# Kernel tuning notes

Hardware: AMD Instinct MI355X
Metric: run time of the kernel (lower is better)

Reference implementation:

```python
import jax, jax.numpy as jnp
import numpy as np

BN_EPS = 1e-5


def feature_gather(fmap, xy):
    """Bilinear grid_sample (align_corners=False, zero padding).
    fmap: (B, C, H, W), xy: (B, N, 2) in [-1, 1]. Returns (B, C, N)."""
    B, C, H, W = fmap.shape
    ix = ((xy[..., 0] + 1.0) * W - 1.0) * 0.5  # (B, N)
    iy = ((xy[..., 1] + 1.0) * H - 1.0) * 0.5
    ix0 = jnp.floor(ix); iy0 = jnp.floor(iy)
    ix1 = ix0 + 1.0;     iy1 = iy0 + 1.0
    wx1 = ix - ix0; wx0 = 1.0 - wx1
    wy1 = iy - iy0; wy0 = 1.0 - wy1

    def corner(fx, fy, w):
        valid = (fx >= 0) & (fx < W) & (fy >= 0) & (fy < H)
        xi = jnp.clip(fx, 0, W - 1).astype(jnp.int32)
        yi = jnp.clip(fy, 0, H - 1).astype(jnp.int32)
        # per-batch fancy gather: (C, H, W)[:, yi, xi] -> (C, N)
        vals = jax.vmap(lambda f, y, x: f[:, y, x])(fmap, yi, xi)  # (B, C, N)
        return vals * (w * valid.astype(fmap.dtype))[:, None, :]

    return (corner(ix0, iy0, wx0 * wy0) + corner(ix1, iy0, wx1 * wy0)
            + corner(ix0, iy1, wx0 * wy1) + corner(ix1, iy1, wx1 * wy1))


def bn1d(x, g, b, m, v):
    # x: (B, C, N); eval-mode batchnorm with running stats
    inv = jax.lax.rsqrt(v + BN_EPS)
    return (x - m[None, :, None]) * (g * inv)[None, :, None] + b[None, :, None]


def setup_inputs() -> dict:
    key = jax.random.key(0)
    ks = jax.random.split(key, 24)
    B, IC, PC, RC, OUT, H, W, N = 64, 32, 128, 32, 128, 96, 320, 2048
    s = 0.1
    return {
        "img_map": jax.random.normal(ks[0], (B, IC, H, W), jnp.float32),
        "xy": jax.random.uniform(ks[1], (B, N, 2), jnp.float32, -1.0, 1.0),
        "point_feas": jax.random.normal(ks[2], (B, PC, N), jnp.float32),
        "W_ia_conv": jax.random.normal(ks[3], (PC, IC), jnp.float32) * s,
        "b_ia_conv": jnp.zeros((PC,), jnp.float32),
        "g1": jnp.ones((PC,), jnp.float32),
        "bt1": jnp.zeros((PC,), jnp.float32),
        "m1": jax.random.normal(ks[4], (PC,), jnp.float32) * s,
        "v1": jax.random.uniform(ks[5], (PC,), jnp.float32, 0.5, 1.5),
        "Wf1": jax.random.normal(ks[6], (RC, IC), jnp.float32) * s,
        "bf1": jnp.zeros((RC,), jnp.float32),
        "Wf2": jax.random.normal(ks[7], (RC, PC), jnp.float32) * s,
        "bf2": jnp.zeros((RC,), jnp.float32),
        "Wf3": jax.random.normal(ks[8], (1, RC), jnp.float32) * s,
        "bf3": jnp.zeros((1,), jnp.float32),
        "W_fuse": jax.random.normal(ks[9], (OUT, 2 * PC), jnp.float32) * s,
        "b_fuse": jnp.zeros((OUT,), jnp.float32),
        "g2": jnp.ones((OUT,), jnp.float32),
        "bt2": jnp.zeros((OUT,), jnp.float32),
        "m2": jax.random.normal(ks[10], (OUT,), jnp.float32) * s,
        "v2": jax.random.uniform(ks[11], (OUT,), jnp.float32, 0.5, 1.5),
    }


def reference(img_map, xy, point_feas, W_ia_conv, b_ia_conv, g1, bt1, m1, v1,
              Wf1, bf1, Wf2, bf2, Wf3, bf3, W_fuse, b_fuse, g2, bt2, m2, v2):
    # Feature_Gather: sample image features at projected point locations
    img_feas = feature_gather(img_map, xy)  # (B, IC, N)

    # IA_Layer attention gate
    ri = jnp.einsum('bin,ri->brn', img_feas, Wf1) + bf1[None, :, None]
    rp = jnp.einsum('bpn,rp->brn', point_feas, Wf2) + bf2[None, :, None]
    att = jax.nn.sigmoid(jnp.einsum('brn,or->bon', jnp.tanh(ri + rp), Wf3)
                         + bf3[None, :, None])  # (B, 1, N)

    # IA_Layer conv1: 1x1 conv IC->PC + BN + ReLU, gated by attention
    img_new = jnp.einsum('bin,pi->bpn', img_feas, W_ia_conv) + b_ia_conv[None, :, None]
    img_new = jax.nn.relu(bn1d(img_new, g1, bt1, m1, v1)) * att  # (B, PC, N)

    # Atten_Fusion_Conv: concat + 1x1 conv + BN + ReLU
    fus = jnp.concatenate([point_feas, img_new], axis=1)  # (B, 2*PC, N)
    fus = jnp.einsum('bcn,oc->bon', fus, W_fuse) + b_fuse[None, :, None]
    return jax.nn.relu(bn1d(fus, g2, bt2, m2, v2))  # (B, OUT, N)
```

## Files before the change

### kernel.cpp

```cpp
#include <hip/hip_runtime.h>
#include <math.h>

constexpr int B    = 64;
constexpr int IC   = 32;
constexpr int PC   = 128;
constexpr int RC   = 32;
constexpr int OUTC = 128;
constexpr int H    = 96;
constexpr int IW   = 320;
constexpr int NPT  = 2048;
constexpr float EPS = 1e-5f;

constexpr int BDIM = 256;
constexpr int NT   = 64;

__device__ __forceinline__ float fast_tanh(float v) {
    float e = __expf(2.f * v);
    return 1.f - 2.f / (e + 1.f);
}
__device__ __forceinline__ float fast_sigmoid(float v) {
    return 1.f / (1.f + __expf(-v));
}

__global__ __launch_bounds__(BDIM, 2) void rcnn_fused(
    const float* __restrict__ img_map, const float* __restrict__ xy,
    const float* __restrict__ point_feas,
    const float* __restrict__ Wia, const float* __restrict__ b_ia,
    const float* __restrict__ g1, const float* __restrict__ bt1,
    const float* __restrict__ m1, const float* __restrict__ v1,
    const float* __restrict__ Wf1, const float* __restrict__ bf1,
    const float* __restrict__ Wf2, const float* __restrict__ bf2,
    const float* __restrict__ Wf3, const float* __restrict__ bf3,
    const float* __restrict__ Wfuse, const float* __restrict__ b_fuse,
    const float* __restrict__ g2, const float* __restrict__ bt2,
    const float* __restrict__ m2, const float* __restrict__ v2,
    float* __restrict__ out)
{
    __shared__ float s_if[NT][IC + 1];
    __shared__ float s_Ximg[PC][NT];
    __shared__ float s_Xpf[32][NT];
    __shared__ float s_Wt[32][OUTC + 4];
    __shared__ float s_attp[4][NT];

    const int t  = threadIdx.x;
    const int b  = blockIdx.y;
    const int n0 = blockIdx.x * NT;
    const int p  = t & 63;
    const int q  = t >> 6;
    const int qu = __builtin_amdgcn_readfirstlane(q);
    const int n  = n0 + p;

    {
        float xc = xy[((size_t)b * NPT + n) * 2 + 0];
        float yc = xy[((size_t)b * NPT + n) * 2 + 1];
        float ix = ((xc + 1.f) * (float)IW - 1.f) * 0.5f;
        float iy = ((yc + 1.f) * (float)H  - 1.f) * 0.5f;
        float fx0 = floorf(ix), fy0 = floorf(iy);
        float wx1 = ix - fx0, wx0f = 1.f - wx1;
        float wy1 = iy - fy0, wy0f = 1.f - wy1;
        int x0 = (int)fx0, y0 = (int)fy0;
        int x1 = x0 + 1,  y1 = y0 + 1;
        bool vx0 = (x0 >= 0) && (x0 < IW), vx1 = (x1 >= 0) && (x1 < IW);
        bool vy0 = (y0 >= 0) && (y0 < H),  vy1 = (y1 >= 0) && (y1 < H);
        int cx0 = min(max(x0, 0), IW - 1), cx1 = min(max(x1, 0), IW - 1);
        int cy0 = min(max(y0, 0), H - 1),  cy1 = min(max(y1, 0), H - 1);
        float w00 = wx0f * wy0f * ((vx0 && vy0) ? 1.f : 0.f);
        float w01 = wx1  * wy0f * ((vx1 && vy0) ? 1.f : 0.f);
        float w10 = wx0f * wy1  * ((vx0 && vy1) ? 1.f : 0.f);
        float w11 = wx1  * wy1  * ((vx1 && vy1) ? 1.f : 0.f);
        int o00 = cy0 * IW + cx0, o01 = cy0 * IW + cx1;
        int o10 = cy1 * IW + cx0, o11 = cy1 * IW + cx1;
        const float* fm = img_map + (size_t)b * IC * H * IW + (size_t)(qu * 8) * (H * IW);
        #pragma unroll
        for (int cc = 0; cc < 8; ++cc) {
            const float* f = fm + (size_t)cc * (H * IW);
            s_if[p][qu * 8 + cc] = w00 * f[o00] + w01 * f[o01] + w10 * f[o10] + w11 * f[o11];
        }
    }
    __syncthreads();

    float fre[IC];
    #pragma unroll
    for (int c = 0; c < IC; ++c) fre[c] = s_if[p][c];

    float racc[8];
    #pragma unroll
    for (int i = 0; i < 8; ++i) racc[i] = bf1[qu * 8 + i] + bf2[qu * 8 + i];
    {
        const float* pfb = point_feas + (size_t)b * PC * NPT + n;
        #pragma unroll 4
        for (int c = 0; c < PC; ++c) {
            float pf = pfb[(size_t)c * NPT];
            #pragma unroll
            for (int i = 0; i < 8; ++i)
                racc[i] += Wf2[(qu * 8 + i) * PC + c] * pf;
        }
    }
    #pragma unroll
    for (int c = 0; c < IC; ++c) {
        #pragma unroll
        for (int i = 0; i < 8; ++i)
            racc[i] += Wf1[(qu * 8 + i) * IC + c] * fre[c];
    }
    {
        float apart = 0.f;
        #pragma unroll
        for (int i = 0; i < 8; ++i) apart += Wf3[qu * 8 + i] * fast_tanh(racc[i]);
        s_attp[q][p] = apart;
    }
    __syncthreads();

    {
        float att = fast_sigmoid(s_attp[0][p] + s_attp[1][p] + s_attp[2][p] + s_attp[3][p]
                                 + bf3[0]);
        #pragma unroll
        for (int oo = 0; oo < 32; ++oo) {
            int o = qu * 32 + oo;
            float acc = 0.f;
            #pragma unroll
            for (int c = 0; c < IC; ++c) acc += Wia[o * IC + c] * fre[c];
            float sc  = g1[o] * rsqrtf(v1[o] + EPS);
            float val = (acc + b_ia[o] - m1[o]) * sc + bt1[o];
            s_Ximg[o][p] = fmaxf(val, 0.f) * att;
        }
    }

    const int tn  = t & 15;
    const int to  = t >> 4;
    const int oo0 = to * 8, nn0 = tn * 4;
    float acc[8][4];
    #pragma unroll
    for (int i = 0; i < 8; ++i)
        #pragma unroll
        for (int k = 0; k < 4; ++k) acc[i][k] = 0.f;

    for (int chk = 0; chk < 8; ++chk) {
        const int cb = chk * 32;
        #pragma unroll
        for (int j = 0; j < 16; ++j) {
            int idx = t + j * BDIM;
            int c = idx & 31, o = idx >> 5;
            s_Wt[c][o] = Wfuse[o * 256 + cb + c];
        }
        if (cb < PC) {
            #pragma unroll
            for (int j = 0; j < 8; ++j) {
                int idx = t + j * BDIM;
                int c = idx >> 6, pp = idx & 63;
                s_Xpf[c][pp] = point_feas[((size_t)b * PC + cb + c) * NPT + n0 + pp];
            }
        }
        __syncthreads();

        const float* Xb = (cb < PC) ? &s_Xpf[0][0] : &s_Ximg[cb - PC][0];
        #pragma unroll 4
        for (int c = 0; c < 32; ++c) {
            float4 xv = *(const float4*)(Xb + c * NT + nn0);
            float4 wa = *(const float4*)(&s_Wt[c][oo0]);
            float4 wb = *(const float4*)(&s_Wt[c][oo0 + 4]);
            float wv[8] = {wa.x, wa.y, wa.z, wa.w, wb.x, wb.y, wb.z, wb.w};
            float xr[4] = {xv.x, xv.y, xv.z, xv.w};
            #pragma unroll
            for (int i = 0; i < 8; ++i)
                #pragma unroll
                for (int k = 0; k < 4; ++k)
                    acc[i][k] += wv[i] * xr[k];
        }
        __syncthreads();
    }

    #pragma unroll
    for (int i = 0; i < 8; ++i) {
        int o = oo0 + i;
        float sc = g2[o] * rsqrtf(v2[o] + EPS);
        float bs = (b_fuse[o] - m2[o]) * sc + bt2[o];
        float4 r;
        r.x = fmaxf(acc[i][0] * sc + bs, 0.f);
        r.y = fmaxf(acc[i][1] * sc + bs, 0.f);
        r.z = fmaxf(acc[i][2] * sc + bs, 0.f);
        r.w = fmaxf(acc[i][3] * sc + bs, 0.f);
        *(float4*)(out + ((size_t)b * OUTC + o) * NPT + n0 + nn0) = r;
    }
}

extern "C" void kernel_launch(void* const* d_in, const int* in_sizes, int n_in,
                              void* d_out, int out_size, void* d_ws, size_t ws_size,
                              hipStream_t stream) {
    const float* img_map    = (const float*)d_in[0];
    const float* xy         = (const float*)d_in[1];
    const float* point_feas = (const float*)d_in[2];
    const float* Wia        = (const float*)d_in[3];
    const float* b_ia       = (const float*)d_in[4];
    const float* g1         = (const float*)d_in[5];
    const float* bt1        = (const float*)d_in[6];
    const float* m1         = (const float*)d_in[7];
    const float* v1         = (const float*)d_in[8];
    const float* Wf1        = (const float*)d_in[9];
    const float* bf1        = (const float*)d_in[10];
    const float* Wf2        = (const float*)d_in[11];
    const float* bf2        = (const float*)d_in[12];
    const float* Wf3        = (const float*)d_in[13];
    const float* bf3        = (const float*)d_in[14];
    const float* Wfuse      = (const float*)d_in[15];
    const float* b_fuse     = (const float*)d_in[16];
    const float* g2         = (const float*)d_in[17];
    const float* bt2        = (const float*)d_in[18];
    const float* m2         = (const float*)d_in[19];
    const float* v2         = (const float*)d_in[20];
    float* out = (float*)d_out;

    dim3 grid(NPT / NT, B);
    rcnn_fused<<<grid, BDIM, 0, stream>>>(
        img_map, xy, point_feas, Wia, b_ia, g1, bt1, m1, v1,
        Wf1, bf1, Wf2, bf2, Wf3, bf3, Wfuse, b_fuse, g2, bt2, m2, v2, out);
}
```

Before: 680.8 us.

## Run fusion GEMM on bf16 MFMA with overlapped shared memory and XCD-aware block mapping

Replaces the FP32 scalar-FMA fusion GEMM with bf16 MFMA 16x16x32 instructions. Weights, point features and gated image features are converted to bf16 and stored in shared memory, and several buffers now share one overlay region to cut LDS use. Launch bounds are raised to allow more resident blocks, and the grid is flattened with a mapping that sends each batch to a single XCD for L2 locality. The BN2 scale and bias are precomputed once into shared memory. Rounding GEMM inputs to bf16 reduces precision, and the output stores are now scalar and strided per lane rather than float4.

```diff
diff --git a/kernel.cpp b/kernel.cpp
--- a/kernel.cpp
+++ b/kernel.cpp
@@ -1,10 +1,12 @@
 #include <hip/hip_runtime.h>
 #include <math.h>
+
+typedef __attribute__((ext_vector_type(8))) short short8;
+typedef __attribute__((ext_vector_type(4))) float floatx4;
 
 constexpr int B    = 64;
 constexpr int IC   = 32;
 constexpr int PC   = 128;
-constexpr int RC   = 32;
 constexpr int OUTC = 128;
 constexpr int H    = 96;
 constexpr int IW   = 320;
@@ -14,6 +16,11 @@
 constexpr int BDIM = 256;
 constexpr int NT   = 64;
 
+__device__ __forceinline__ unsigned f2bf(float x) {
+    unsigned u = __builtin_bit_cast(unsigned, x);
+    u += 0x7FFFu + ((u >> 16) & 1u);
+    return u >> 16;
+}
 __device__ __forceinline__ float fast_tanh(float v) {
     float e = __expf(2.f * v);
     return 1.f - 2.f / (e + 1.f);
@@ -22,7 +29,7 @@
     return 1.f / (1.f + __expf(-v));
 }
 
-__global__ __launch_bounds__(BDIM, 2) void rcnn_fused(
+__global__ __launch_bounds__(BDIM, 4) void rcnn_fused(
     const float* __restrict__ img_map, const float* __restrict__ xy,
     const float* __restrict__ point_feas,
     const float* __restrict__ Wia, const float* __restrict__ b_ia,
@@ -36,19 +43,31 @@
     const float* __restrict__ m2, const float* __restrict__ v2,
     float* __restrict__ out)
 {
-    __shared__ float s_if[NT][IC + 1];
-    __shared__ float s_Ximg[PC][NT];
-    __shared__ float s_Xpf[32][NT];
-    __shared__ float s_Wt[32][OUTC + 4];
-    __shared__ float s_attp[4][NT];
-
-    const int t  = threadIdx.x;
-    const int b  = blockIdx.y;
-    const int n0 = blockIdx.x * NT;
-    const int p  = t & 63;
-    const int q  = t >> 6;
-    const int qu = __builtin_amdgcn_readfirstlane(q);
-    const int n  = n0 + p;
+    __shared__ __align__(16) short s_Ximg[NT][136];
+    __shared__ __align__(16) char s_ovl[15360];
+    __shared__ float s_sc[OUTC], s_bs[OUTC];
+
+    short (*s_Wc)[40]  = (short(*)[40])s_ovl;
+    short (*s_Xpf)[40] = (short(*)[40])(s_ovl + 10240);
+    float (*s_if)[33]  = (float(*)[33])s_ovl;
+    float (*s_attp)[NT]= (float(*)[NT])(s_ovl + 8448);
+
+    const int t    = threadIdx.x;
+    const int bid  = blockIdx.x;
+    const int xcd  = bid & 7;
+    const int rr   = bid >> 3;
+    const int b    = (xcd << 3) | (rr >> 5);
+    const int n0   = (rr & 31) * NT;
+    const int lane = t & 63;
+    const int w    = t >> 6;
+    const int wq   = __builtin_amdgcn_readfirstlane(w);
+    const int n    = n0 + lane;
+
+    if (t < OUTC) {
+        float sc = g2[t] * rsqrtf(v2[t] + EPS);
+        s_sc[t] = sc;
+        s_bs[t] = (b_fuse[t] - m2[t]) * sc + bt2[t];
+    }
 
     {
         float xc = xy[((size_t)b * NPT + n) * 2 + 0];
@@ -70,116 +89,125 @@
         float w11 = wx1  * wy1  * ((vx1 && vy1) ? 1.f : 0.f);
         int o00 = cy0 * IW + cx0, o01 = cy0 * IW + cx1;
         int o10 = cy1 * IW + cx0, o11 = cy1 * IW + cx1;
-        const float* fm = img_map + (size_t)b * IC * H * IW + (size_t)(qu * 8) * (H * IW);
+        const float* fm = img_map + (size_t)b * IC * H * IW + (size_t)(wq * 8) * (H * IW);
         #pragma unroll
         for (int cc = 0; cc < 8; ++cc) {
             const float* f = fm + (size_t)cc * (H * IW);
-            s_if[p][qu * 8 + cc] = w00 * f[o00] + w01 * f[o01] + w10 * f[o10] + w11 * f[o11];
+            s_if[lane][wq * 8 + cc] = w00 * f[o00] + w01 * f[o01] + w10 * f[o10] + w11 * f[o11];
         }
     }
     __syncthreads();
 
     float fre[IC];
     #pragma unroll
-    for (int c = 0; c < IC; ++c) fre[c] = s_if[p][c];
-
-    float racc[8];
-    #pragma unroll
-    for (int i = 0; i < 8; ++i) racc[i] = bf1[qu * 8 + i] + bf2[qu * 8 + i];
+    for (int c = 0; c < IC; ++c) fre[c] = s_if[lane][c];
+
     {
+        float racc[8];
+        #pragma unroll
+        for (int i = 0; i < 8; ++i) racc[i] = bf1[wq * 8 + i] + bf2[wq * 8 + i];
         const float* pfb = point_feas + (size_t)b * PC * NPT + n;
         #pragma unroll 4
         for (int c = 0; c < PC; ++c) {
             float pf = pfb[(size_t)c * NPT];
             #pragma unroll
             for (int i = 0; i < 8; ++i)
-                racc[i] += Wf2[(qu * 8 + i) * PC + c] * pf;
-        }
-    }
+                racc[i] += Wf2[(wq * 8 + i) * PC + c] * pf;
+        }
+        #pragma unroll
+        for (int c = 0; c < IC; ++c) {
+            #pragma unroll
+            for (int i = 0; i < 8; ++i)
+                racc[i] += Wf1[(wq * 8 + i) * IC + c] * fre[c];
+        }
+        float apart = 0.f;
+        #pragma unroll
+        for (int i = 0; i < 8; ++i) apart += Wf3[wq * 8 + i] * fast_tanh(racc[i]);
+        s_attp[w][lane] = apart;
+    }
+    __syncthreads();
+
+    {
+        float att = fast_sigmoid(s_attp[0][lane] + s_attp[1][lane] + s_attp[2][lane]
+                                 + s_attp[3][lane] + bf3[0]);
+        #pragma unroll
+        for (int jj = 0; jj < 4; ++jj) {
+            short8 v;
+            #pragma unroll
+            for (int e = 0; e < 8; ++e) {
+                int o = wq * 32 + jj * 8 + e;
+                float acc = 0.f;
+                #pragma unroll
+                for (int c = 0; c < IC; ++c) acc += Wia[o * IC + c] * fre[c];
+                float sc  = g1[o] * rsqrtf(v1[o] + EPS);
+                float val = (acc + b_ia[o] - m1[o]) * sc + bt1[o];
+                val = fmaxf(val, 0.f) * att;
+                v[e] = (short)f2bf(val);
+            }
+            *(short8*)&s_Ximg[lane][wq * 32 + jj * 8] = v;
+        }
+    }
+    __syncthreads();
+
+    const int row16 = lane & 15;
+    const int quad  = lane >> 4;
+    floatx4 acc[2][4];
     #pragma unroll
-    for (int c = 0; c < IC; ++c) {
-        #pragma unroll
-        for (int i = 0; i < 8; ++i)
-            racc[i] += Wf1[(qu * 8 + i) * IC + c] * fre[c];
-    }
-    {
-        float apart = 0.f;
-        #pragma unroll
-        for (int i = 0; i < 8; ++i) apart += Wf3[qu * 8 + i] * fast_tanh(racc[i]);
-        s_attp[q][p] = apart;
-    }
-    __syncthreads();
-
-    {
-        float att = fast_sigmoid(s_attp[0][p] + s_attp[1][p] + s_attp[2][p] + s_attp[3][p]
-                                 + bf3[0]);
-        #pragma unroll
-        for (int oo = 0; oo < 32; ++oo) {
-            int o = qu * 32 + oo;
-            float acc = 0.f;
-            #pragma unroll
-            for (int c = 0; c < IC; ++c) acc += Wia[o * IC + c] * fre[c];
-            float sc  = g1[o] * rsqrtf(v1[o] + EPS);
-            float val = (acc + b_ia[o] - m1[o]) * sc + bt1[o];
-            s_Ximg[o][p] = fmaxf(val, 0.f) * att;
-        }
-    }
-
-    const int tn  = t & 15;
-    const int to  = t >> 4;
-    const int oo0 = to * 8, nn0 = tn * 4;
-    float acc[8][4];
+    for (int mt = 0; mt < 2; ++mt)
+        #pragma unroll
+        for (int nt = 0; nt < 4; ++nt) acc[mt][nt] = (floatx4){0.f, 0.f, 0.f, 0.f};
+
+    for (int chk = 0; chk < 8; ++chk) {
+        const int k0 = chk * 32;
+        #pragma unroll
+        for (int j = 0; j < 8; ++j) {
+            int idx = j * 256 + t;
+            int c2 = (idx & 15) * 2, o = idx >> 4;
+            float2 wv = *(const float2*)&Wfuse[o * 256 + k0 + c2];
+            *(unsigned*)&s_Wc[o][c2] = f2bf(wv.x) | (f2bf(wv.y) << 16);
+        }
+        if (chk < 4) {
+            #pragma unroll
+            for (int j = 0; j < 4; ++j) {
+                int idx = j * 256 + t;
+                int n2 = (idx & 31) * 2, c = idx >> 5;
+                float2 pv = *(const float2*)&point_feas[((size_t)b * PC + k0 + c) * NPT + n0 + n2];
+                s_Xpf[n2][c]     = (short)f2bf(pv.x);
+                s_Xpf[n2 + 1][c] = (short)f2bf(pv.y);
+            }
+        }
+        __syncthreads();
+
+        short8 afr[2], bfr[4];
+        #pragma unroll
+        for (int mt = 0; mt < 2; ++mt)
+            afr[mt] = *(const short8*)&s_Wc[wq * 32 + mt * 16 + row16][quad * 8];
+        #pragma unroll
+        for (int nt = 0; nt < 4; ++nt) {
+            const short* src = (chk < 4) ? &s_Xpf[nt * 16 + row16][quad * 8]
+                                         : &s_Ximg[nt * 16 + row16][(chk - 4) * 32 + quad * 8];
+            bfr[nt] = *(const short8*)src;
+        }
+        #pragma unroll
+        for (int mt = 0; mt < 2; ++mt)
+            #pragma unroll
+            for (int nt = 0; nt < 4; ++nt)
+                acc[mt][nt] = __builtin_amdgcn_mfma_f32_16x16x32_bf16(
+                                  afr[mt], bfr[nt], acc[mt][nt], 0, 0, 0);
+        if (chk != 7) __syncthreads();
+    }
+
     #pragma unroll
-    for (int i = 0; i < 8; ++i)
-        #pragma unroll
-        for (int k = 0; k < 4; ++k) acc[i][k] = 0.f;
-
-    for (int chk = 0; chk < 8; ++chk) {
-        const int cb = chk * 32;
-        #pragma unroll
-        for (int j = 0; j < 16; ++j) {
-            int idx = t + j * BDIM;
-            int c = idx & 31, o = idx >> 5;
-            s_Wt[c][o] = Wfuse[o * 256 + cb + c];
-        }
-        if (cb < PC) {
-            #pragma unroll
-            for (int j = 0; j < 8; ++j) {
-                int idx = t + j * BDIM;
-                int c = idx >> 6, pp = idx & 63;
-                s_Xpf[c][pp] = point_feas[((size_t)b * PC + cb + c) * NPT + n0 + pp];
+    for (int mt = 0; mt < 2; ++mt) {
+        #pragma unroll
+        for (int nt = 0; nt < 4; ++nt) {
+            #pragma unroll
+            for (int r2 = 0; r2 < 4; ++r2) {
+                int o = wq * 32 + mt * 16 + quad * 4 + r2;
+                float val = fmaxf(acc[mt][nt][r2] * s_sc[o] + s_bs[o], 0.f);
+                out[((size_t)b * OUTC + o) * NPT + n0 + nt * 16 + row16] = val;
             }
         }
-        __syncthreads();
-
-        const float* Xb = (cb < PC) ? &s_Xpf[0][0] : &s_Ximg[cb - PC][0];
-        #pragma unroll 4
-        for (int c = 0; c < 32; ++c) {
-            float4 xv = *(const float4*)(Xb + c * NT + nn0);
-            float4 wa = *(const float4*)(&s_Wt[c][oo0]);
-            float4 wb = *(const float4*)(&s_Wt[c][oo0 + 4]);
-            float wv[8] = {wa.x, wa.y, wa.z, wa.w, wb.x, wb.y, wb.z, wb.w};
-            float xr[4] = {xv.x, xv.y, xv.z, xv.w};
-            #pragma unroll
-            for (int i = 0; i < 8; ++i)
-                #pragma unroll
-                for (int k = 0; k < 4; ++k)
-                    acc[i][k] += wv[i] * xr[k];
-        }
-        __syncthreads();
-    }
-
-    #pragma unroll
-    for (int i = 0; i < 8; ++i) {
-        int o = oo0 + i;
-        float sc = g2[o] * rsqrtf(v2[o] + EPS);
-        float bs = (b_fuse[o] - m2[o]) * sc + bt2[o];
-        float4 r;
-        r.x = fmaxf(acc[i][0] * sc + bs, 0.f);
-        r.y = fmaxf(acc[i][1] * sc + bs, 0.f);
-        r.z = fmaxf(acc[i][2] * sc + bs, 0.f);
-        r.w = fmaxf(acc[i][3] * sc + bs, 0.f);
-        *(float4*)(out + ((size_t)b * OUTC + o) * NPT + n0 + nn0) = r;
     }
 }
 
@@ -209,8 +237,7 @@
     const float* v2         = (const float*)d_in[20];
     float* out = (float*)d_out;
 
-    dim3 grid(NPT / NT, B);
-    rcnn_fused<<<grid, BDIM, 0, stream>>>(
+    rcnn_fused<<<dim3(2048), BDIM, 0, stream>>>(
         img_map, xy, point_feas, Wia, b_ia, g1, bt1, m1, v1,
         Wf1, bf1, Wf2, bf2, Wf3, bf3, Wfuse, b_fuse, g2, bt2, m2, v2, out);
 }
```

Measured after the change: 567.9 us. 1.2x faster.
